# Performance work log

Measured on AMD Instinct MI355X. Metric: run time of the kernel, lower is better.

## Reference

```python
import jax, jax.numpy as jnp
import numpy as np

B = 32768          # batch
NA = 8             # n_agents
A = NA - 1         # other agents
OBS = 64
ACT = 14
OTH_IN = 82        # (sum(obs)+sum(act)-obs_i+act_i)//(NA-1)
H_SELF = 64
H_OTH = 128
H2 = 64
HEADS = 4
AD = H_OTH // HEADS  # 32
MAX_ACTION = 1.0
SCALE = float(np.sqrt(AD))


def setup_inputs() -> dict:
    key = jax.random.key(0)
    ks = jax.random.split(key, 24)
    r = jax.random.normal
    u = jax.random.uniform
    inp = {
        "state_one": r(ks[0], (B, OBS), jnp.float32),
        "act_one": u(ks[1], (B, ACT), jnp.float32),
        "state_others": r(ks[2], (A, B, OBS), jnp.float32),
        "act_others": u(ks[3], (A, B, OTH_IN - OBS), jnp.float32),
        # self encoder
        "W1": r(ks[4], (OBS + ACT, H_SELF), jnp.float32) * 0.05,
        "b1": r(ks[5], (H_SELF,), jnp.float32) * 0.05,
        "W2": r(ks[6], (H_SELF, H_SELF), jnp.float32) * 0.05,
        "b2": r(ks[7], (H_SELF,), jnp.float32) * 0.05,
        "w3_self": r(ks[8], (H_SELF, H2), jnp.float32) * 0.01,  # init.normal_(0, 0.01)
        # per-other-agent encoders (stacked ModuleList)
        "We": r(ks[9], (A, OTH_IN, H_OTH), jnp.float32) * 0.05,
        "be": r(ks[10], (A, H_OTH), jnp.float32) * 0.05,
        # attention heads (stacked)
        "Wk": r(ks[11], (HEADS, H_OTH, AD), jnp.float32) * 0.05,   # no bias
        "Wq": r(ks[12], (HEADS, H_SELF, AD), jnp.float32) * 0.05,  # no bias
        "Wv": r(ks[13], (HEADS, H_OTH, AD), jnp.float32) * 0.05,
        "bv": r(ks[14], (HEADS, AD), jnp.float32) * 0.05,
        "w3_others": r(ks[15], (H_OTH, H2), jnp.float32) * 0.01,
        "Wout": r(ks[16], (H2, 1), jnp.float32) * 0.05,
        "bout": r(ks[17], (1,), jnp.float32) * 0.05,
    }
    return inp


def reference(state_one, act_one, state_others, act_others,
              W1, b1, W2, b2, w3_self, We, be,
              Wk, Wq, Wv, bv, w3_others, Wout, bout):
    act_one = act_one / MAX_ACTION
    act_others = act_others / MAX_ACTION

    # self branch
    x = jnp.concatenate([state_one, act_one], axis=-1)          # [B, 78]
    x1 = jax.nn.relu(x @ W1 + b1)                               # [B, 64]
    x2 = jax.nn.relu(x1 @ W2 + b2)                              # [B, 64]
    x3_self = x2 @ w3_self                                      # [B, 64]

    # per-other-agent encoders
    inps = jnp.concatenate([state_others, act_others], axis=-1)  # [A, B, 82]
    enc = jax.nn.relu(jnp.einsum('abi,aij->abj', inps, We) + be[:, None, :])  # [A, B, 128]

    # multi-head attention: query from x1 (self), keys/values from encodings
    keys = jnp.einsum('abj,hjd->habd', enc, Wk)                  # [H, A, B, d]
    vals = jax.nn.relu(jnp.einsum('abj,hjd->habd', enc, Wv) + bv[:, None, None, :])
    sel = jnp.einsum('bj,hjd->hbd', x1, Wq)                      # [H, B, d]
    logits = jnp.einsum('hbd,habd->hba', sel, keys) / SCALE      # [H, B, A]
    w = jax.nn.softmax(logits, axis=-1)
    ov = jnp.einsum('habd,hba->hbd', vals, w)                    # [H, B, d]

    # concat heads along feature dim (head-major, as torch.cat over head list)
    x2_others = jnp.transpose(ov, (1, 0, 2)).reshape(-1, HEADS * AD)  # [B, 128]
    x3_others = x2_others @ w3_others                            # [B, 64]

    x3 = jax.nn.relu(x3_self + x3_others)
    return x3 @ Wout + bout                                      # [B, 1]
```

## Files before the change

kernel.cpp:

```cpp
#include <hip/hip_runtime.h>
#include <hip/hip_bf16.h>

#define BTOT 32768
#define TB 32

typedef __attribute__((ext_vector_type(8))) short bhalf8;
typedef __attribute__((ext_vector_type(4))) float f32x4;

static __device__ __forceinline__ unsigned short f2bf(float x) {
    __hip_bfloat16 h = __float2bfloat16(x);
    unsigned short u;
    __builtin_memcpy(&u, &h, sizeof(u));
    return u;
}
static __device__ __forceinline__ float bf2f(unsigned short s) {
    return __uint_as_float(((unsigned int)s) << 16);
}
static __device__ __forceinline__ float bflo(unsigned int u) {
    return __uint_as_float(u << 16);
}
static __device__ __forceinline__ float bfhi(unsigned int u) {
    return __uint_as_float(u & 0xffff0000u);
}

__global__ __launch_bounds__(256) void fold_M_frag(
        const float* __restrict__ Wk, const float* __restrict__ Wq,
        unsigned short* __restrict__ Mf2)
{
    int tid = blockIdx.x * 256 + threadIdx.x;
    int h  = tid >> 13;
    int jq = (tid >> 7) & 63;
    int j  = tid & 127;
    const float* q = Wq + (h*64 + jq)*32;
    const float* k = Wk + (h*128 + j)*32;
    float acc = 0.f;
#pragma unroll
    for (int d = 0; d < 32; d += 4) {
        float4 a = *(const float4*)(q + d);
        float4 b = *(const float4*)(k + d);
        acc += a.x*b.x + a.y*b.y + a.z*b.z + a.w*b.w;
    }
    unsigned short hi = f2bf(acc);
    unsigned short lo = f2bf(acc - bf2f(hi));
    int n  = h*128 + j;
    int kt = jq >> 5, qd = (jq >> 3) & 3, jj = jq & 7;
    int nt = n >> 4,  ln = n & 15;
    size_t base = (((nt*2 + kt)*64) + qd*16 + ln)*16;
    Mf2[base + jj]     = hi;
    Mf2[base + 8 + jj] = lo;
}

__global__ __launch_bounds__(256) void conv_We(
        const float* __restrict__ We, unsigned short* __restrict__ Wef2)
{
    int tid = blockIdx.x * 256 + threadIdx.x;
    int a = tid / 12288;
    int r = tid - a*12288;
    int k = r >> 7;
    int n = r & 127;
    float v = (k < 82) ? We[((size_t)a*82 + k)*128 + n] : 0.f;
    unsigned short hi = f2bf(v);
    unsigned short lo = f2bf(v - bf2f(hi));
    int kt = k >> 5, qd = (k >> 3) & 3, j = k & 7;
    int nt = n >> 4, ln = n & 15;
    size_t base = (size_t)a*24576 + (((nt*3 + kt)*64) + qd*16 + ln)*16;
    Wef2[base + j]     = hi;
    Wef2[base + 8 + j] = lo;
}

__global__ __launch_bounds__(256) void conv_Wv(
        const float* __restrict__ Wv, unsigned short* __restrict__ Wvf2)
{
    int tid = blockIdx.x * 256 + threadIdx.x;
    int h = tid >> 12;
    int j = (tid >> 5) & 127;
    int d = tid & 31;
    float v = Wv[tid];
    unsigned short hi = f2bf(v);
    unsigned short lo = f2bf(v - bf2f(hi));
    int k = j, n = h*32 + d;
    int kt = k >> 5, qd = (k >> 3) & 3, jj = k & 7;
    int nt = n >> 4, ln = n & 15;
    size_t base = (((nt*4 + kt)*64) + qd*16 + ln)*16;
    Wvf2[base + jj]     = hi;
    Wvf2[base + 8 + jj] = lo;
}

__global__ __launch_bounds__(256) void conv_self(
        const float* __restrict__ W2, const float* __restrict__ w3_self,
        const float* __restrict__ w3_others,
        unsigned short* __restrict__ W2f, unsigned short* __restrict__ w3sf,
        unsigned short* __restrict__ w3of)
{
    int tid = blockIdx.x * 256 + threadIdx.x;
    const float* src;
    unsigned short* dst;
    int idx, KT;
    if (tid < 4096)       { src = W2;        dst = W2f;  idx = tid;        KT = 2; }
    else if (tid < 8192)  { src = w3_self;   dst = w3sf; idx = tid - 4096; KT = 2; }
    else                  { src = w3_others; dst = w3of; idx = tid - 8192; KT = 4; }
    int k = idx >> 6;
    int n = idx & 63;
    float v = src[k*64 + n];
    unsigned short hi = f2bf(v);
    unsigned short lo = f2bf(v - bf2f(hi));
    int kt = k >> 5, qd = (k >> 3) & 3, j = k & 7;
    int nt = n >> 4, ln = n & 15;
    size_t base = (((nt*KT + kt)*64) + qd*16 + ln)*16;
    dst[base + j]     = hi;
    dst[base + 8 + j] = lo;
}

__global__ __launch_bounds__(256, 2) void fused_critic(
    const float* __restrict__ state_one, const float* __restrict__ act_one,
    const float* __restrict__ state_others, const float* __restrict__ act_others,
    const float* __restrict__ W1, const float* __restrict__ b1,
    const float* __restrict__ b2, const float* __restrict__ be,
    const float* __restrict__ bvp, const float* __restrict__ Wout,
    const float* __restrict__ bout,
    const unsigned short* __restrict__ Mf2, const unsigned short* __restrict__ Wef2,
    const unsigned short* __restrict__ Wvf2, const unsigned short* __restrict__ W2f,
    const unsigned short* __restrict__ w3sf, const unsigned short* __restrict__ w3of,
    float* __restrict__ out)
{
    __shared__ __align__(16) unsigned char smem[61440];
    float*          sX    = (float*)smem;
    unsigned short* sX1bH = (unsigned short*)(smem + 10752);
    unsigned short* sX1bL = (unsigned short*)(smem + 15360);
    unsigned short* sX2bH = (unsigned short*)(smem + 19968);
    unsigned short* sX2bL = (unsigned short*)(smem + 24576);
    unsigned short* sT    = (unsigned short*)smem;
    unsigned short* sOvH  = (unsigned short*)smem;
    unsigned short* sOvL  = (unsigned short*)(smem + 8704);
    float*          sRed  = (float*)(smem + 17408);

    const int t  = threadIdx.x;
    const int b0 = blockIdx.x * TB;
    const int w  = t >> 6;
    const int l  = t & 63;
    const int m  = l & 15;
    const int qd = l >> 4;

    const int act_r = t >> 3, act_c = t & 7;

    auto stageIn = [&](unsigned short* dH, unsigned short* dL,
                       const float4& vA, const float4& vB, const float* av) {
        const int r0 = t >> 4, c4 = (t & 15) << 2;
        ushort4 h4, l4;
        h4.x = f2bf(vA.x); l4.x = f2bf(vA.x - bf2f(h4.x));
        h4.y = f2bf(vA.y); l4.y = f2bf(vA.y - bf2f(h4.y));
        h4.z = f2bf(vA.z); l4.z = f2bf(vA.z - bf2f(h4.z));
        h4.w = f2bf(vA.w); l4.w = f2bf(vA.w - bf2f(h4.w));
        *(ushort4*)(dH + r0*104 + c4) = h4;
        *(ushort4*)(dL + r0*104 + c4) = l4;
        h4.x = f2bf(vB.x); l4.x = f2bf(vB.x - bf2f(h4.x));
        h4.y = f2bf(vB.y); l4.y = f2bf(vB.y - bf2f(h4.y));
        h4.z = f2bf(vB.z); l4.z = f2bf(vB.z - bf2f(h4.z));
        h4.w = f2bf(vB.w); l4.w = f2bf(vB.w - bf2f(h4.w));
        *(ushort4*)(dH + (r0+16)*104 + c4) = h4;
        *(ushort4*)(dL + (r0+16)*104 + c4) = l4;
        if (act_c < 6) {
#pragma unroll
            for (int e = 0; e < 3; ++e) {
                float v = av[e];
                unsigned short hh = f2bf(v);
                dH[act_r*104 + 64 + act_c*3 + e] = hh;
                dL[act_r*104 + 64 + act_c*3 + e] = f2bf(v - bf2f(hh));
            }
        }
    };

    for (int f = t; f < TB*16; f += 256) {
        int r = f >> 4, c4 = (f & 15) << 2;
        *(float4*)(sX + r*84 + c4) =
            *(const float4*)(state_one + (size_t)(b0 + r)*64 + c4);
    }
    for (int f = t; f < TB*14; f += 256) {
        int r = f / 14, c = f - r*14;
        sX[r*84 + 64 + c] = act_one[(size_t)(b0 + r)*14 + c];
    }
    __syncthreads();

    const int cg = t & 15, rg = t >> 4;
    const int c0 = cg << 2;

    {
        float acc[2][4] = {};
#pragma unroll 2
        for (int k = 0; k < 78; ++k) {
            float4 wv = *(const float4*)(W1 + k*64 + c0);
            float a0 = sX[(rg*2+0)*84 + k];
            float a1 = sX[(rg*2+1)*84 + k];
            acc[0][0] += a0*wv.x; acc[0][1] += a0*wv.y; acc[0][2] += a0*wv.z; acc[0][3] += a0*wv.w;
            acc[1][0] += a1*wv.x; acc[1][1] += a1*wv.y; acc[1][2] += a1*wv.z; acc[1][3] += a1*wv.w;
        }
        float4 bb = *(const float4*)(b1 + c0);
#pragma unroll
        for (int i = 0; i < 2; ++i) {
            int r = rg*2 + i;
            float v[4];
            v[0] = fmaxf(acc[i][0] + bb.x, 0.f);
            v[1] = fmaxf(acc[i][1] + bb.y, 0.f);
            v[2] = fmaxf(acc[i][2] + bb.z, 0.f);
            v[3] = fmaxf(acc[i][3] + bb.w, 0.f);
#pragma unroll
            for (int e = 0; e < 4; ++e) {
                unsigned short hh = f2bf(v[e]);
                sX1bH[r*72 + c0+e] = hh;
                sX1bL[r*72 + c0+e] = f2bf(v[e] - bf2f(hh));
            }
        }
    }
    __syncthreads();

    {
        f32x4 acc2[2] = {};
#pragma unroll
        for (int kt = 0; kt < 2; ++kt) {
            bhalf8 ah0 = *(const bhalf8*)(sX1bH + m*72      + kt*32 + qd*8);
            bhalf8 ah1 = *(const bhalf8*)(sX1bH + (16+m)*72 + kt*32 + qd*8);
            bhalf8 al0 = *(const bhalf8*)(sX1bL + m*72      + kt*32 + qd*8);
            bhalf8 al1 = *(const bhalf8*)(sX1bL + (16+m)*72 + kt*32 + qd*8);
            const unsigned short* bp = W2f + ((w*2 + kt)*64 + l)*16;
            bhalf8 bh = *(const bhalf8*)(bp);
            bhalf8 bl = *(const bhalf8*)(bp + 8);
            acc2[0] = __builtin_amdgcn_mfma_f32_16x16x32_bf16(ah0, bh, acc2[0], 0, 0, 0);
            acc2[1] = __builtin_amdgcn_mfma_f32_16x16x32_bf16(ah1, bh, acc2[1], 0, 0, 0);
            acc2[0] = __builtin_amdgcn_mfma_f32_16x16x32_bf16(ah0, bl, acc2[0], 0, 0, 0);
            acc2[1] = __builtin_amdgcn_mfma_f32_16x16x32_bf16(ah1, bl, acc2[1], 0, 0, 0);
            acc2[0] = __builtin_amdgcn_mfma_f32_16x16x32_bf16(al0, bh, acc2[0], 0, 0, 0);
            acc2[1] = __builtin_amdgcn_mfma_f32_16x16x32_bf16(al1, bh, acc2[1], 0, 0, 0);
        }
        int col = w*16 + m;
        float b2c = b2[col];
#pragma unroll
        for (int rt = 0; rt < 2; ++rt)
#pragma unroll
            for (int r = 0; r < 4; ++r) {
                float e = fmaxf(acc2[rt][r] + b2c, 0.f);
                int row = rt*16 + qd*4 + r;
                unsigned short hh = f2bf(e);
                sX2bH[row*72 + col] = hh;
                sX2bL[row*72 + col] = f2bf(e - bf2f(hh));
            }
    }
    __syncthreads();

    f32x4 x3a[2] = {};
    {
#pragma unroll
        for (int kt = 0; kt < 2; ++kt) {
            bhalf8 ah0 = *(const bhalf8*)(sX2bH + m*72      + kt*32 + qd*8);
            bhalf8 ah1 = *(const bhalf8*)(sX2bH + (16+m)*72 + kt*32 + qd*8);
            bhalf8 al0 = *(const bhalf8*)(sX2bL + m*72      + kt*32 + qd*8);
            bhalf8 al1 = *(const bhalf8*)(sX2bL + (16+m)*72 + kt*32 + qd*8);
            const unsigned short* bp = w3sf + ((w*2 + kt)*64 + l)*16;
            bhalf8 bh = *(const bhalf8*)(bp);
            bhalf8 bl = *(const bhalf8*)(bp + 8);
            x3a[0] = __builtin_amdgcn_mfma_f32_16x16x32_bf16(ah0, bh, x3a[0], 0, 0, 0);
            x3a[1] = __builtin_amdgcn_mfma_f32_16x16x32_bf16(ah1, bh, x3a[1], 0, 0, 0);
            x3a[0] = __builtin_amdgcn_mfma_f32_16x16x32_bf16(ah0, bl, x3a[0], 0, 0, 0);
            x3a[1] = __builtin_amdgcn_mfma_f32_16x16x32_bf16(ah1, bl, x3a[1], 0, 0, 0);
            x3a[0] = __builtin_amdgcn_mfma_f32_16x16x32_bf16(al0, bh, x3a[0], 0, 0, 0);
            x3a[1] = __builtin_amdgcn_mfma_f32_16x16x32_bf16(al1, bh, x3a[1], 0, 0, 0);
        }
    }

    {
        f32x4 tacc[2][8] = {};
#pragma unroll
        for (int kt = 0; kt < 2; ++kt) {
            bhalf8 ah0 = *(const bhalf8*)(sX1bH + m*72      + kt*32 + qd*8);
            bhalf8 ah1 = *(const bhalf8*)(sX1bH + (16+m)*72 + kt*32 + qd*8);
            bhalf8 al0 = *(const bhalf8*)(sX1bL + m*72      + kt*32 + qd*8);
            bhalf8 al1 = *(const bhalf8*)(sX1bL + (16+m)*72 + kt*32 + qd*8);
#pragma unroll
            for (int nt2 = 0; nt2 < 8; ++nt2) {
                int nt = w*8 + nt2;
                const unsigned short* bp = Mf2 + ((nt*2 + kt)*64 + l)*16;
                bhalf8 bh = *(const bhalf8*)(bp);
                bhalf8 bl = *(const bhalf8*)(bp + 8);
                tacc[0][nt2] = __builtin_amdgcn_mfma_f32_16x16x32_bf16(ah0, bh, tacc[0][nt2], 0, 0, 0);
                tacc[1][nt2] = __builtin_amdgcn_mfma_f32_16x16x32_bf16(ah1, bh, tacc[1][nt2], 0, 0, 0);
                tacc[0][nt2] = __builtin_amdgcn_mfma_f32_16x16x32_bf16(ah0, bl, tacc[0][nt2], 0, 0, 0);
                tacc[1][nt2] = __builtin_amdgcn_mfma_f32_16x16x32_bf16(ah1, bl, tacc[1][nt2], 0, 0, 0);
                tacc[0][nt2] = __builtin_amdgcn_mfma_f32_16x16x32_bf16(al0, bh, tacc[0][nt2], 0, 0, 0);
                tacc[1][nt2] = __builtin_amdgcn_mfma_f32_16x16x32_bf16(al1, bh, tacc[1][nt2], 0, 0, 0);
            }
        }
        __syncthreads();
#pragma unroll
        for (int rt = 0; rt < 2; ++rt)
#pragma unroll
            for (int nt2 = 0; nt2 < 8; ++nt2)
#pragma unroll
                for (int r = 0; r < 4; ++r)
                    sT[(rt*16 + qd*4 + r)*520 + w*128 + nt2*16 + m] =
                        f2bf(tacc[rt][nt2][r]);
    }
    __syncthreads();

    const int b_l = l & 31, half = l >> 5;
    uint4 tq[8];
    {
        const uint4* tp4 = (const uint4*)(sT + b_l*520 + w*128 + half*64);
#pragma unroll
        for (int i = 0; i < 8; ++i) tq[i] = tp4[i];
    }
    __syncthreads();

    for (int f = t; f < TB*16; f += 256) {
        int r = f >> 4, c = f & 15;
        if (c >= 2) {
#pragma unroll
            for (int k = 0; k < 2; ++k) {
                unsigned short* dH = (unsigned short*)(smem + k*13312);
                unsigned short* dL = (unsigned short*)(smem + k*13312 + 6656);
                dH[r*104 + 80 + c] = 0;
                dL[r*104 + 80 + c] = 0;
            }
        }
    }
    {
        const float* sa = state_others + (size_t)b0 * 64;
        float4 vA = *(const float4*)(sa + t*4);
        float4 vB = *(const float4*)(sa + t*4 + 1024);
        float av[3] = {0.f, 0.f, 0.f};
        if (act_c < 6) {
            const float* aa = act_others + (size_t)(b0 + act_r)*18 + act_c*3;
            av[0] = aa[0]; av[1] = aa[1]; av[2] = aa[2];
        }
        stageIn((unsigned short*)smem, (unsigned short*)(smem + 6656),
                vA, vB, av);
    }
    __syncthreads();

    const float bv0 = bvp[w*32 + m];
    const float bv1 = bvp[w*32 + 16 + m];
    f32x4 o4[2][2] = {};
    float mR = -1e30f, sR = 0.f;

    float4 pfA, pfB; float pfa[3] = {0.f, 0.f, 0.f};

    for (int a = 0; a < 7; ++a) {
        unsigned short* sInHc = (unsigned short*)(smem + (a&1)*13312);
        unsigned short* sInLc = (unsigned short*)(smem + (a&1)*13312 + 6656);
        unsigned short* sEnHc = (unsigned short*)(smem + 26624 + (a&1)*17408);
        unsigned short* sEnLc = (unsigned short*)(smem + 26624 + (a&1)*17408 + 8704);
        unsigned short* sInHn = (unsigned short*)(smem + ((a+1)&1)*13312);
        unsigned short* sInLn = (unsigned short*)(smem + ((a+1)&1)*13312 + 6656);

        if (a < 6) {
            const float* sa = state_others + ((size_t)(a+1)*BTOT + b0)*64;
            pfA = *(const float4*)(sa + t*4);
            pfB = *(const float4*)(sa + t*4 + 1024);
            if (act_c < 6) {
                const float* aa = act_others
                    + ((size_t)(a+1)*BTOT + b0 + act_r)*18 + act_c*3;
                pfa[0] = aa[0]; pfa[1] = aa[1]; pfa[2] = aa[2];
            }
        }
        float be0 = be[a*128 + 32*w + m];
        float be1 = be[a*128 + 32*w + 16 + m];

        f32x4 eacc[2][2] = {};
#pragma unroll
        for (int kt = 0; kt < 3; ++kt) {
            bhalf8 ah0 = *(const bhalf8*)(sInHc + m*104      + kt*32 + qd*8);
            bhalf8 ah1 = *(const bhalf8*)(sInHc + (16+m)*104 + kt*32 + qd*8);
            bhalf8 al0 = *(const bhalf8*)(sInLc + m*104      + kt*32 + qd*8);
            bhalf8 al1 = *(const bhalf8*)(sInLc + (16+m)*104 + kt*32 + qd*8);
#pragma unroll
            for (int nt2 = 0; nt2 < 2; ++nt2) {
                int nt = 2*w + nt2;
                const unsigned short* bp =
                    Wef2 + (size_t)a*24576 + ((nt*3 + kt)*64 + l)*16;
                bhalf8 bh = *(const bhalf8*)(bp);
                bhalf8 bl = *(const bhalf8*)(bp + 8);
                eacc[0][nt2] = __builtin_amdgcn_mfma_f32_16x16x32_bf16(ah0, bh, eacc[0][nt2], 0, 0, 0);
                eacc[1][nt2] = __builtin_amdgcn_mfma_f32_16x16x32_bf16(ah1, bh, eacc[1][nt2], 0, 0, 0);
                eacc[0][nt2] = __builtin_amdgcn_mfma_f32_16x16x32_bf16(ah0, bl, eacc[0][nt2], 0, 0, 0);
                eacc[1][nt2] = __builtin_amdgcn_mfma_f32_16x16x32_bf16(ah1, bl, eacc[1][nt2], 0, 0, 0);
                eacc[0][nt2] = __builtin_amdgcn_mfma_f32_16x16x32_bf16(al0, bh, eacc[0][nt2], 0, 0, 0);
                eacc[1][nt2] = __builtin_amdgcn_mfma_f32_16x16x32_bf16(al1, bh, eacc[1][nt2], 0, 0, 0);
            }
        }

        {
#pragma unroll
            for (int rt = 0; rt < 2; ++rt)
#pragma unroll
                for (int nt2 = 0; nt2 < 2; ++nt2) {
                    float bb = nt2 ? be1 : be0;
#pragma unroll
                    for (int r = 0; r < 4; ++r) {
                        float e = fmaxf(eacc[rt][nt2][r] + bb, 0.f);
                        int row = rt*16 + qd*4 + r;
                        int col = 32*w + nt2*16 + m;
                        unsigned short hh = f2bf(e);
                        sEnHc[row*136 + col] = hh;
                        sEnLc[row*136 + col] = f2bf(e - bf2f(hh));
                    }
                }
        }
        if (a < 6) stageIn(sInHn, sInLn, pfA, pfB, pfa);

        __syncthreads();

        float alpha, pp;
        {
            const uint4* ehp = (const uint4*)(sEnHc + b_l*136 + half*64);
            const uint4* elp = (const uint4*)(sEnLc + b_l*136 + half*64);
            float part = 0.f;
#pragma unroll
            for (int i = 0; i < 8; ++i) {
                uint4 eh = ehp[i];
                uint4 el = elp[i];
                uint4 tt = tq[i];
                part += (bflo(eh.x)+bflo(el.x))*bflo(tt.x)
                      + (bfhi(eh.x)+bfhi(el.x))*bfhi(tt.x);
                part += (bflo(eh.y)+bflo(el.y))*bflo(tt.y)
                      + (bfhi(eh.y)+bfhi(el.y))*bfhi(tt.y);
                part += (bflo(eh.z)+bflo(el.z))*bflo(tt.z)
                      + (bfhi(eh.z)+bfhi(el.z))*bfhi(tt.z);
                part += (bflo(eh.w)+bflo(el.w))*bflo(tt.w)
                      + (bfhi(eh.w)+bfhi(el.w))*bfhi(tt.w);
            }
            part += __shfl_xor(part, 32);
            float lg = part * 0.17677669529663687f;
            float mn = fmaxf(mR, lg);
            alpha = __expf(mR - mn);
            pp    = __expf(lg - mn);
            sR = sR*alpha + pp;
            mR = mn;
        }

        {
            f32x4 vacc[2][2] = {};
#pragma unroll
            for (int kt = 0; kt < 4; ++kt) {
                bhalf8 ah0 = *(const bhalf8*)(sEnHc + m*136      + kt*32 + qd*8);
                bhalf8 ah1 = *(const bhalf8*)(sEnHc + (16+m)*136 + kt*32 + qd*8);
                bhalf8 al0 = *(const bhalf8*)(sEnLc + m*136      + kt*32 + qd*8);
                bhalf8 al1 = *(const bhalf8*)(sEnLc + (16+m)*136 + kt*32 + qd*8);
#pragma unroll
                for (int nt2 = 0; nt2 < 2; ++nt2) {
                    int nt = 2*w + nt2;
                    const unsigned short* bp = Wvf2 + ((nt*4 + kt)*64 + l)*16;
                    bhalf8 bh = *(const bhalf8*)(bp);
                    bhalf8 bl = *(const bhalf8*)(bp + 8);
                    vacc[0][nt2] = __builtin_amdgcn_mfma_f32_16x16x32_bf16(ah0, bh, vacc[0][nt2], 0, 0, 0);
                    vacc[1][nt2] = __builtin_amdgcn_mfma_f32_16x16x32_bf16(ah1, bh, vacc[1][nt2], 0, 0, 0);
                    vacc[0][nt2] = __builtin_amdgcn_mfma_f32_16x16x32_bf16(ah0, bl, vacc[0][nt2], 0, 0, 0);
                    vacc[1][nt2] = __builtin_amdgcn_mfma_f32_16x16x32_bf16(ah1, bl, vacc[1][nt2], 0, 0, 0);
                    vacc[0][nt2] = __builtin_amdgcn_mfma_f32_16x16x32_bf16(al0, bh, vacc[0][nt2], 0, 0, 0);
                    vacc[1][nt2] = __builtin_amdgcn_mfma_f32_16x16x32_bf16(al1, bh, vacc[1][nt2], 0, 0, 0);
                }
            }
#pragma unroll
            for (int rt = 0; rt < 2; ++rt)
#pragma unroll
                for (int r = 0; r < 4; ++r) {
                    int row = rt*16 + qd*4 + r;
                    float al = __shfl(alpha, row);
                    float p  = __shfl(pp, row);
#pragma unroll
                    for (int nt2 = 0; nt2 < 2; ++nt2) {
                        float bb = nt2 ? bv1 : bv0;
                        o4[rt][nt2][r] = o4[rt][nt2][r]*al
                                       + p*fmaxf(vacc[rt][nt2][r] + bb, 0.f);
                    }
                }
        }
    }
    __syncthreads();

    {
        float rinv = 1.0f / sR;
#pragma unroll
        for (int rt = 0; rt < 2; ++rt)
#pragma unroll
            for (int r = 0; r < 4; ++r) {
                int row = rt*16 + qd*4 + r;
                float inv = __shfl(rinv, row);
#pragma unroll
                for (int nt2 = 0; nt2 < 2; ++nt2) {
                    float v = o4[rt][nt2][r]*inv;
                    int col = 32*w + nt2*16 + m;
                    unsigned short hh = f2bf(v);
                    sOvH[row*136 + col] = hh;
                    sOvL[row*136 + col] = f2bf(v - bf2f(hh));
                }
            }
    }
    __syncthreads();

    {
#pragma unroll
        for (int kt = 0; kt < 4; ++kt) {
            bhalf8 ah0 = *(const bhalf8*)(sOvH + m*136      + kt*32 + qd*8);
            bhalf8 ah1 = *(const bhalf8*)(sOvH + (16+m)*136 + kt*32 + qd*8);
            bhalf8 al0 = *(const bhalf8*)(sOvL + m*136      + kt*32 + qd*8);
            bhalf8 al1 = *(const bhalf8*)(sOvL + (16+m)*136 + kt*32 + qd*8);
            const unsigned short* bp = w3of + ((w*4 + kt)*64 + l)*16;
            bhalf8 bh = *(const bhalf8*)(bp);
            bhalf8 bl = *(const bhalf8*)(bp + 8);
            x3a[0] = __builtin_amdgcn_mfma_f32_16x16x32_bf16(ah0, bh, x3a[0], 0, 0, 0);
            x3a[1] = __builtin_amdgcn_mfma_f32_16x16x32_bf16(ah1, bh, x3a[1], 0, 0, 0);
            x3a[0] = __builtin_amdgcn_mfma_f32_16x16x32_bf16(ah0, bl, x3a[0], 0, 0, 0);
            x3a[1] = __builtin_amdgcn_mfma_f32_16x16x32_bf16(ah1, bl, x3a[1], 0, 0, 0);
            x3a[0] = __builtin_amdgcn_mfma_f32_16x16x32_bf16(al0, bh, x3a[0], 0, 0, 0);
            x3a[1] = __builtin_amdgcn_mfma_f32_16x16x32_bf16(al1, bh, x3a[1], 0, 0, 0);
        }
        float wo = Wout[w*16 + m];
#pragma unroll
        for (int rt = 0; rt < 2; ++rt)
#pragma unroll
            for (int r = 0; r < 4; ++r) {
                float p = fmaxf(x3a[rt][r], 0.f) * wo;
                p += __shfl_xor(p, 1);
                p += __shfl_xor(p, 2);
                p += __shfl_xor(p, 4);
                p += __shfl_xor(p, 8);
                if (m == 0)
                    sRed[(rt*16 + qd*4 + r)*4 + w] = p;
            }
    }
    __syncthreads();
    if (t < 32)
        out[b0 + t] = sRed[t*4+0] + sRed[t*4+1] + sRed[t*4+2] + sRed[t*4+3]
                    + bout[0];
}

extern "C" void kernel_launch(void* const* d_in, const int* in_sizes, int n_in,
                              void* d_out, int out_size, void* d_ws, size_t ws_size,
                              hipStream_t stream) {
    (void)in_sizes; (void)n_in; (void)out_size; (void)ws_size;
    const float* state_one    = (const float*)d_in[0];
    const float* act_one      = (const float*)d_in[1];
    const float* state_others = (const float*)d_in[2];
    const float* act_others   = (const float*)d_in[3];
    const float* W1           = (const float*)d_in[4];
    const float* b1           = (const float*)d_in[5];
    const float* W2           = (const float*)d_in[6];
    const float* b2           = (const float*)d_in[7];
    const float* w3_self      = (const float*)d_in[8];
    const float* We           = (const float*)d_in[9];
    const float* be           = (const float*)d_in[10];
    const float* Wk           = (const float*)d_in[11];
    const float* Wq           = (const float*)d_in[12];
    const float* Wv           = (const float*)d_in[13];
    const float* bv           = (const float*)d_in[14];
    const float* w3_others    = (const float*)d_in[15];
    const float* Wout         = (const float*)d_in[16];
    const float* bout         = (const float*)d_in[17];
    float* out = (float*)d_out;

    unsigned short* Mf2  = (unsigned short*)d_ws;
    unsigned short* Wef2 = (unsigned short*)((char*)d_ws + 131072);
    unsigned short* Wvf2 = (unsigned short*)((char*)d_ws + 475136);
    unsigned short* W2f  = (unsigned short*)((char*)d_ws + 540672);
    unsigned short* w3sf = (unsigned short*)((char*)d_ws + 557056);
    unsigned short* w3of = (unsigned short*)((char*)d_ws + 573440);

    fold_M_frag<<<128, 256, 0, stream>>>(Wk, Wq, Mf2);
    conv_We<<<336, 256, 0, stream>>>(We, Wef2);
    conv_Wv<<<64, 256, 0, stream>>>(Wv, Wvf2);
    conv_self<<<64, 256, 0, stream>>>(W2, w3_self, w3_others, W2f, w3sf, w3of);
    fused_critic<<<BTOT/TB, 256, 0, stream>>>(
        state_one, act_one, state_others, act_others,
        W1, b1, b2, be, bv, Wout, bout,
        Mf2, Wef2, Wvf2, W2f, w3sf, w3of, out);
}
```

Before: 233.8 us.

## Move first self layer and attention logits onto split-bf16 MFMA

The first self-encoder layer (x @ W1) now runs on 16x16x32 bf16 MFMA with hi/lo split operands instead of a scalar FP32 loop. W1 is pre-converted into fragment layout by the existing weight-conversion kernel. The per-agent attention logit dot products are also computed with MFMA against the folded key-query matrix, sharing the encoding fragments already loaded for the value projection, and the results are gathered with lane selects and shuffles. This removes VALU work and scalar LDS traffic, at the cost of the small errors from the three-term bf16 split and some extra shuffles.

```diff
diff --git a/kernel.cpp b/kernel.cpp
--- a/kernel.cpp
+++ b/kernel.cpp
@@ -15,12 +15,6 @@
 }
 static __device__ __forceinline__ float bf2f(unsigned short s) {
     return __uint_as_float(((unsigned int)s) << 16);
-}
-static __device__ __forceinline__ float bflo(unsigned int u) {
-    return __uint_as_float(u << 16);
-}
-static __device__ __forceinline__ float bfhi(unsigned int u) {
-    return __uint_as_float(u & 0xffff0000u);
 }
 
 __global__ __launch_bounds__(256) void fold_M_frag(
@@ -88,20 +82,22 @@
 
 __global__ __launch_bounds__(256) void conv_self(
         const float* __restrict__ W2, const float* __restrict__ w3_self,
-        const float* __restrict__ w3_others,
+        const float* __restrict__ w3_others, const float* __restrict__ W1,
         unsigned short* __restrict__ W2f, unsigned short* __restrict__ w3sf,
-        unsigned short* __restrict__ w3of)
+        unsigned short* __restrict__ w3of, unsigned short* __restrict__ W1f)
 {
     int tid = blockIdx.x * 256 + threadIdx.x;
+    if (tid >= 22528) return;
     const float* src;
     unsigned short* dst;
-    int idx, KT;
-    if (tid < 4096)       { src = W2;        dst = W2f;  idx = tid;        KT = 2; }
-    else if (tid < 8192)  { src = w3_self;   dst = w3sf; idx = tid - 4096; KT = 2; }
-    else                  { src = w3_others; dst = w3of; idx = tid - 8192; KT = 4; }
+    int idx, KT, kmax;
+    if (tid < 4096)       { src = W2;        dst = W2f;  idx = tid;         KT = 2; kmax = 64; }
+    else if (tid < 8192)  { src = w3_self;   dst = w3sf; idx = tid - 4096;  KT = 2; kmax = 64; }
+    else if (tid < 16384) { src = w3_others; dst = w3of; idx = tid - 8192;  KT = 4; kmax = 128; }
+    else                  { src = W1;        dst = W1f;  idx = tid - 16384; KT = 3; kmax = 78; }
     int k = idx >> 6;
     int n = idx & 63;
-    float v = src[k*64 + n];
+    float v = (k < kmax) ? src[k*64 + n] : 0.f;
     unsigned short hi = f2bf(v);
     unsigned short lo = f2bf(v - bf2f(hi));
     int kt = k >> 5, qd = (k >> 3) & 3, j = k & 7;
@@ -114,21 +110,21 @@
 __global__ __launch_bounds__(256, 2) void fused_critic(
     const float* __restrict__ state_one, const float* __restrict__ act_one,
     const float* __restrict__ state_others, const float* __restrict__ act_others,
-    const float* __restrict__ W1, const float* __restrict__ b1,
-    const float* __restrict__ b2, const float* __restrict__ be,
-    const float* __restrict__ bvp, const float* __restrict__ Wout,
-    const float* __restrict__ bout,
+    const float* __restrict__ b1, const float* __restrict__ b2,
+    const float* __restrict__ be, const float* __restrict__ bvp,
+    const float* __restrict__ Wout, const float* __restrict__ bout,
     const unsigned short* __restrict__ Mf2, const unsigned short* __restrict__ Wef2,
     const unsigned short* __restrict__ Wvf2, const unsigned short* __restrict__ W2f,
     const unsigned short* __restrict__ w3sf, const unsigned short* __restrict__ w3of,
-    float* __restrict__ out)
+    const unsigned short* __restrict__ W1f, float* __restrict__ out)
 {
     __shared__ __align__(16) unsigned char smem[61440];
-    float*          sX    = (float*)smem;
-    unsigned short* sX1bH = (unsigned short*)(smem + 10752);
-    unsigned short* sX1bL = (unsigned short*)(smem + 15360);
-    unsigned short* sX2bH = (unsigned short*)(smem + 19968);
-    unsigned short* sX2bL = (unsigned short*)(smem + 24576);
+    unsigned short* sXbH  = (unsigned short*)smem;
+    unsigned short* sXbL  = (unsigned short*)(smem + 6656);
+    unsigned short* sX1bH = (unsigned short*)(smem + 13312);
+    unsigned short* sX1bL = (unsigned short*)(smem + 17920);
+    unsigned short* sX2bH = (unsigned short*)(smem + 22528);
+    unsigned short* sX2bL = (unsigned short*)(smem + 27136);
     unsigned short* sT    = (unsigned short*)smem;
     unsigned short* sOvH  = (unsigned short*)smem;
     unsigned short* sOvL  = (unsigned short*)(smem + 8704);
@@ -170,46 +166,69 @@
         }
     };
 
-    for (int f = t; f < TB*16; f += 256) {
-        int r = f >> 4, c4 = (f & 15) << 2;
-        *(float4*)(sX + r*84 + c4) =
-            *(const float4*)(state_one + (size_t)(b0 + r)*64 + c4);
-    }
-    for (int f = t; f < TB*14; f += 256) {
-        int r = f / 14, c = f - r*14;
-        sX[r*84 + 64 + c] = act_one[(size_t)(b0 + r)*14 + c];
-    }
-    __syncthreads();
-
-    const int cg = t & 15, rg = t >> 4;
-    const int c0 = cg << 2;
-
-    {
-        float acc[2][4] = {};
-#pragma unroll 2
-        for (int k = 0; k < 78; ++k) {
-            float4 wv = *(const float4*)(W1 + k*64 + c0);
-            float a0 = sX[(rg*2+0)*84 + k];
-            float a1 = sX[(rg*2+1)*84 + k];
-            acc[0][0] += a0*wv.x; acc[0][1] += a0*wv.y; acc[0][2] += a0*wv.z; acc[0][3] += a0*wv.w;
-            acc[1][0] += a1*wv.x; acc[1][1] += a1*wv.y; acc[1][2] += a1*wv.z; acc[1][3] += a1*wv.w;
-        }
-        float4 bb = *(const float4*)(b1 + c0);
-#pragma unroll
-        for (int i = 0; i < 2; ++i) {
-            int r = rg*2 + i;
-            float v[4];
-            v[0] = fmaxf(acc[i][0] + bb.x, 0.f);
-            v[1] = fmaxf(acc[i][1] + bb.y, 0.f);
-            v[2] = fmaxf(acc[i][2] + bb.z, 0.f);
-            v[3] = fmaxf(acc[i][3] + bb.w, 0.f);
-#pragma unroll
-            for (int e = 0; e < 4; ++e) {
-                unsigned short hh = f2bf(v[e]);
-                sX1bH[r*72 + c0+e] = hh;
-                sX1bL[r*72 + c0+e] = f2bf(v[e] - bf2f(hh));
-            }
-        }
+    {
+        const int r0 = t >> 4, c4 = (t & 15) << 2;
+        float4 vA = *(const float4*)(state_one + (size_t)(b0 + r0)*64 + c4);
+        float4 vB = *(const float4*)(state_one + (size_t)(b0 + r0 + 16)*64 + c4);
+        ushort4 h4, l4;
+        h4.x = f2bf(vA.x); l4.x = f2bf(vA.x - bf2f(h4.x));
+        h4.y = f2bf(vA.y); l4.y = f2bf(vA.y - bf2f(h4.y));
+        h4.z = f2bf(vA.z); l4.z = f2bf(vA.z - bf2f(h4.z));
+        h4.w = f2bf(vA.w); l4.w = f2bf(vA.w - bf2f(h4.w));
+        *(ushort4*)(sXbH + r0*104 + c4) = h4;
+        *(ushort4*)(sXbL + r0*104 + c4) = l4;
+        h4.x = f2bf(vB.x); l4.x = f2bf(vB.x - bf2f(h4.x));
+        h4.y = f2bf(vB.y); l4.y = f2bf(vB.y - bf2f(h4.y));
+        h4.z = f2bf(vB.z); l4.z = f2bf(vB.z - bf2f(h4.z));
+        h4.w = f2bf(vB.w); l4.w = f2bf(vB.w - bf2f(h4.w));
+        *(ushort4*)(sXbH + (r0+16)*104 + c4) = h4;
+        *(ushort4*)(sXbL + (r0+16)*104 + c4) = l4;
+#pragma unroll
+        for (int e = 0; e < 2; ++e) {
+            int cc = act_c*2 + e;
+            float v = (cc < 14) ? act_one[(size_t)(b0 + act_r)*14 + cc] : 0.f;
+            unsigned short hh = f2bf(v);
+            sXbH[act_r*104 + 64 + cc] = hh;
+            sXbL[act_r*104 + 64 + cc] = f2bf(v - bf2f(hh));
+        }
+        for (int f = t; f < TB*16; f += 256) {
+            int r = f >> 4, c = 80 + (f & 15);
+            sXbH[r*104 + c] = 0;
+            sXbL[r*104 + c] = 0;
+        }
+    }
+    __syncthreads();
+
+    {
+        f32x4 acc1[2] = {};
+#pragma unroll
+        for (int kt = 0; kt < 3; ++kt) {
+            bhalf8 ah0 = *(const bhalf8*)(sXbH + m*104      + kt*32 + qd*8);
+            bhalf8 ah1 = *(const bhalf8*)(sXbH + (16+m)*104 + kt*32 + qd*8);
+            bhalf8 al0 = *(const bhalf8*)(sXbL + m*104      + kt*32 + qd*8);
+            bhalf8 al1 = *(const bhalf8*)(sXbL + (16+m)*104 + kt*32 + qd*8);
+            const unsigned short* bp = W1f + ((w*3 + kt)*64 + l)*16;
+            bhalf8 bh = *(const bhalf8*)(bp);
+            bhalf8 bl = *(const bhalf8*)(bp + 8);
+            acc1[0] = __builtin_amdgcn_mfma_f32_16x16x32_bf16(ah0, bh, acc1[0], 0, 0, 0);
+            acc1[1] = __builtin_amdgcn_mfma_f32_16x16x32_bf16(ah1, bh, acc1[1], 0, 0, 0);
+            acc1[0] = __builtin_amdgcn_mfma_f32_16x16x32_bf16(ah0, bl, acc1[0], 0, 0, 0);
+            acc1[1] = __builtin_amdgcn_mfma_f32_16x16x32_bf16(ah1, bl, acc1[1], 0, 0, 0);
+            acc1[0] = __builtin_amdgcn_mfma_f32_16x16x32_bf16(al0, bh, acc1[0], 0, 0, 0);
+            acc1[1] = __builtin_amdgcn_mfma_f32_16x16x32_bf16(al1, bh, acc1[1], 0, 0, 0);
+        }
+        int col = w*16 + m;
+        float b1c = b1[col];
+#pragma unroll
+        for (int rt = 0; rt < 2; ++rt)
+#pragma unroll
+            for (int r = 0; r < 4; ++r) {
+                float e = fmaxf(acc1[rt][r] + b1c, 0.f);
+                int row = rt*16 + qd*4 + r;
+                unsigned short hh = f2bf(e);
+                sX1bH[row*72 + col] = hh;
+                sX1bL[row*72 + col] = f2bf(e - bf2f(hh));
+            }
     }
     __syncthreads();
 
@@ -300,12 +319,14 @@
     }
     __syncthreads();
 
-    const int b_l = l & 31, half = l >> 5;
-    uint4 tq[8];
-    {
-        const uint4* tp4 = (const uint4*)(sT + b_l*520 + w*128 + half*64);
-#pragma unroll
-        for (int i = 0; i < 8; ++i) tq[i] = tp4[i];
+    const int b_l = l & 31;
+    bhalf8 tB0[4], tB1[4];
+    {
+#pragma unroll
+        for (int kt = 0; kt < 4; ++kt) {
+            tB0[kt] = *(const bhalf8*)(sT + m*520      + w*128 + kt*32 + qd*8);
+            tB1[kt] = *(const bhalf8*)(sT + (16+m)*520 + w*128 + kt*32 + qd*8);
+        }
     }
     __syncthreads();
 
@@ -339,6 +360,9 @@
     const float bv1 = bvp[w*32 + 16 + m];
     f32x4 o4[2][2] = {};
     float mR = -1e30f, sR = 0.f;
+
+    const int nsel = l & 15;
+    const int srcl = ((nsel >> 2) << 4) | nsel;
 
     float4 pfA, pfB; float pfa[3] = {0.f, 0.f, 0.f};
 
@@ -407,26 +431,44 @@
 
         __syncthreads();
 
+        f32x4 vacc[2][2] = {};
+        f32x4 lacc0 = {}, lacc1 = {};
+#pragma unroll
+        for (int kt = 0; kt < 4; ++kt) {
+            bhalf8 ah0 = *(const bhalf8*)(sEnHc + m*136      + kt*32 + qd*8);
+            bhalf8 ah1 = *(const bhalf8*)(sEnHc + (16+m)*136 + kt*32 + qd*8);
+            bhalf8 al0 = *(const bhalf8*)(sEnLc + m*136      + kt*32 + qd*8);
+            bhalf8 al1 = *(const bhalf8*)(sEnLc + (16+m)*136 + kt*32 + qd*8);
+#pragma unroll
+            for (int nt2 = 0; nt2 < 2; ++nt2) {
+                int nt = 2*w + nt2;
+                const unsigned short* bp = Wvf2 + ((nt*4 + kt)*64 + l)*16;
+                bhalf8 bh = *(const bhalf8*)(bp);
+                bhalf8 bl = *(const bhalf8*)(bp + 8);
+                vacc[0][nt2] = __builtin_amdgcn_mfma_f32_16x16x32_bf16(ah0, bh, vacc[0][nt2], 0, 0, 0);
+                vacc[1][nt2] = __builtin_amdgcn_mfma_f32_16x16x32_bf16(ah1, bh, vacc[1][nt2], 0, 0, 0);
+                vacc[0][nt2] = __builtin_amdgcn_mfma_f32_16x16x32_bf16(ah0, bl, vacc[0][nt2], 0, 0, 0);
+                vacc[1][nt2] = __builtin_amdgcn_mfma_f32_16x16x32_bf16(ah1, bl, vacc[1][nt2], 0, 0, 0);
+                vacc[0][nt2] = __builtin_amdgcn_mfma_f32_16x16x32_bf16(al0, bh, vacc[0][nt2], 0, 0, 0);
+                vacc[1][nt2] = __builtin_amdgcn_mfma_f32_16x16x32_bf16(al1, bh, vacc[1][nt2], 0, 0, 0);
+            }
+            lacc0 = __builtin_amdgcn_mfma_f32_16x16x32_bf16(ah0, tB0[kt], lacc0, 0, 0, 0);
+            lacc0 = __builtin_amdgcn_mfma_f32_16x16x32_bf16(al0, tB0[kt], lacc0, 0, 0, 0);
+            lacc1 = __builtin_amdgcn_mfma_f32_16x16x32_bf16(ah1, tB1[kt], lacc1, 0, 0, 0);
+            lacc1 = __builtin_amdgcn_mfma_f32_16x16x32_bf16(al1, tB1[kt], lacc1, 0, 0, 0);
+        }
+
         float alpha, pp;
         {
-            const uint4* ehp = (const uint4*)(sEnHc + b_l*136 + half*64);
-            const uint4* elp = (const uint4*)(sEnLc + b_l*136 + half*64);
-            float part = 0.f;
-#pragma unroll
-            for (int i = 0; i < 8; ++i) {
-                uint4 eh = ehp[i];
-                uint4 el = elp[i];
-                uint4 tt = tq[i];
-                part += (bflo(eh.x)+bflo(el.x))*bflo(tt.x)
-                      + (bfhi(eh.x)+bfhi(el.x))*bfhi(tt.x);
-                part += (bflo(eh.y)+bflo(el.y))*bflo(tt.y)
-                      + (bfhi(eh.y)+bfhi(el.y))*bfhi(tt.y);
-                part += (bflo(eh.z)+bflo(el.z))*bflo(tt.z)
-                      + (bfhi(eh.z)+bfhi(el.z))*bfhi(tt.z);
-                part += (bflo(eh.w)+bflo(el.w))*bflo(tt.w)
-                      + (bfhi(eh.w)+bfhi(el.w))*bfhi(tt.w);
-            }
-            part += __shfl_xor(part, 32);
+            float e01 = (l & 1) ? lacc0[1] : lacc0[0];
+            float e23 = (l & 1) ? lacc0[3] : lacc0[2];
+            float d0  = (l & 2) ? e23 : e01;
+            float f01 = (l & 1) ? lacc1[1] : lacc1[0];
+            float f23 = (l & 1) ? lacc1[3] : lacc1[2];
+            float d1  = (l & 2) ? f23 : f01;
+            float g0 = __shfl(d0, srcl);
+            float g1 = __shfl(d1, srcl);
+            float part = (l & 16) ? g1 : g0;
             float lg = part * 0.17677669529663687f;
             float mn = fmaxf(mR, lg);
             alpha = __expf(mR - mn);
@@ -436,27 +478,6 @@
         }
 
         {
-            f32x4 vacc[2][2] = {};
-#pragma unroll
-            for (int kt = 0; kt < 4; ++kt) {
-                bhalf8 ah0 = *(const bhalf8*)(sEnHc + m*136      + kt*32 + qd*8);
-                bhalf8 ah1 = *(const bhalf8*)(sEnHc + (16+m)*136 + kt*32 + qd*8);
-                bhalf8 al0 = *(const bhalf8*)(sEnLc + m*136      + kt*32 + qd*8);
-                bhalf8 al1 = *(const bhalf8*)(sEnLc + (16+m)*136 + kt*32 + qd*8);
-#pragma unroll
-                for (int nt2 = 0; nt2 < 2; ++nt2) {
-                    int nt = 2*w + nt2;
-                    const unsigned short* bp = Wvf2 + ((nt*4 + kt)*64 + l)*16;
-                    bhalf8 bh = *(const bhalf8*)(bp);
-                    bhalf8 bl = *(const bhalf8*)(bp + 8);
-                    vacc[0][nt2] = __builtin_amdgcn_mfma_f32_16x16x32_bf16(ah0, bh, vacc[0][nt2], 0, 0, 0);
-                    vacc[1][nt2] = __builtin_amdgcn_mfma_f32_16x16x32_bf16(ah1, bh, vacc[1][nt2], 0, 0, 0);
-                    vacc[0][nt2] = __builtin_amdgcn_mfma_f32_16x16x32_bf16(ah0, bl, vacc[0][nt2], 0, 0, 0);
-                    vacc[1][nt2] = __builtin_amdgcn_mfma_f32_16x16x32_bf16(ah1, bl, vacc[1][nt2], 0, 0, 0);
-                    vacc[0][nt2] = __builtin_amdgcn_mfma_f32_16x16x32_bf16(al0, bh, vacc[0][nt2], 0, 0, 0);
-                    vacc[1][nt2] = __builtin_amdgcn_mfma_f32_16x16x32_bf16(al1, bh, vacc[1][nt2], 0, 0, 0);
-                }
-            }
 #pragma unroll
             for (int rt = 0; rt < 2; ++rt)
 #pragma unroll
@@ -562,13 +583,15 @@
     unsigned short* W2f  = (unsigned short*)((char*)d_ws + 540672);
     unsigned short* w3sf = (unsigned short*)((char*)d_ws + 557056);
     unsigned short* w3of = (unsigned short*)((char*)d_ws + 573440);
+    unsigned short* W1f  = (unsigned short*)((char*)d_ws + 606208);
 
     fold_M_frag<<<128, 256, 0, stream>>>(Wk, Wq, Mf2);
     conv_We<<<336, 256, 0, stream>>>(We, Wef2);
     conv_Wv<<<64, 256, 0, stream>>>(Wv, Wvf2);
-    conv_self<<<64, 256, 0, stream>>>(W2, w3_self, w3_others, W2f, w3sf, w3of);
+    conv_self<<<88, 256, 0, stream>>>(W2, w3_self, w3_others, W1,
+                                      W2f, w3sf, w3of, W1f);
     fused_critic<<<BTOT/TB, 256, 0, stream>>>(
         state_one, act_one, state_others, act_others,
-        W1, b1, b2, be, bv, Wout, bout,
-        Mf2, Wef2, Wvf2, W2f, w3sf, w3of, out);
-}
+        b1, b2, be, bv, Wout, bout,
+        Mf2, Wef2, Wvf2, W2f, w3sf, w3of, W1f, out);
+}
```

Result: faster. 207.9 us (-11.1%).
